# Kernel tuning notes

Hardware: AMD Instinct MI355X
Metric: run time of the kernel (lower is better)

## Reference

```python
import jax, jax.numpy as jnp
import numpy as np
import math

B, N, C = 4, 2048, 768
H = 12
DFF = 4 * C
EPS = 1e-5

def _layernorm(x, gamma, beta):
    mu = jnp.mean(x, axis=-1, keepdims=True)
    var = jnp.var(x, axis=-1, keepdims=True)
    return (x - mu) * jax.lax.rsqrt(var + EPS) * gamma + beta

def setup_inputs() -> dict:
    key = jax.random.key(0)
    ks = jax.random.split(key, 12)
    s = 0.02
    return {
        "x": jax.random.normal(ks[0], (B, N, C), jnp.float32),
        "Wqkv": jax.random.normal(ks[1], (C, 3 * C), jnp.float32) * s,
        "bqkv": jnp.zeros((3 * C,), jnp.float32),
        "Wproj": jax.random.normal(ks[2], (C, C), jnp.float32) * s,
        "bproj": jnp.zeros((C,), jnp.float32),
        "g1": jnp.ones((C,), jnp.float32),
        "b1": jnp.zeros((C,), jnp.float32),
        "g2": jnp.ones((C,), jnp.float32),
        "b2": jnp.zeros((C,), jnp.float32),
        "Wfc1": jax.random.normal(ks[3], (C, DFF), jnp.float32) * s,
        "bfc1": jnp.zeros((DFF,), jnp.float32),
        "Wfc2": jax.random.normal(ks[4], (DFF, C), jnp.float32) * s,
        "bfc2": jnp.zeros((C,), jnp.float32),
    }

def reference(x, Wqkv, bqkv, Wproj, bproj, g1, b1, g2, b2, Wfc1, bfc1, Wfc2, bfc2):
    head_dim = C // H
    qkv = x @ Wqkv + bqkv                      # [B,N,3C]
    q, k, v = jnp.split(qkv, 3, axis=-1)
    # [B,N,C] -> [B,H,N,hd]
    def to_heads(t):
        return t.reshape(B, N, H, head_dim).transpose(0, 2, 1, 3)
    q, k, v = to_heads(q), to_heads(k), to_heads(v)
    attn = jnp.einsum('bhqd,bhkd->bhqk', q, k) / math.sqrt(head_dim)
    attn = jax.nn.softmax(attn, axis=-1)       # dropout p=0 -> identity
    out = jnp.einsum('bhqk,bhkd->bhqd', attn, v)
    out = out.transpose(0, 2, 1, 3).reshape(B, N, C)
    out = out @ Wproj + bproj
    x = _layernorm(x + out, g1, b1)
    h = jax.nn.gelu(x @ Wfc1 + bfc1, approximate=False) @ Wfc2 + bfc2
    x = _layernorm(x + h, g2, b2)
    return x
```

## Files before the change

kernel.cpp:

```cpp
#include <hip/hip_runtime.h>

typedef __bf16 bf16;
typedef __bf16 bf16x2 __attribute__((ext_vector_type(2)));
typedef __bf16 bf16x4 __attribute__((ext_vector_type(4)));
typedef __bf16 bf16x8 __attribute__((ext_vector_type(8)));
typedef float  f32x4  __attribute__((ext_vector_type(4)));
typedef float  f32x16 __attribute__((ext_vector_type(16)));
typedef int    intx4  __attribute__((ext_vector_type(4)));

#define BB 4
#define SEQ 2048
#define CH 768
#define NH 12
#define HD 64
#define DFF 3072
#define MROWS (BB * SEQ)
#define C3 (3 * CH)
#define NBH (BB * NH)

__device__ inline f32x16 mfma32(bf16x8 a, bf16x8 b, f32x16 c) {
    return __builtin_amdgcn_mfma_f32_32x32x16_bf16(a, b, c, 0, 0, 0);
}
__device__ inline f32x4 mfma16(bf16x8 a, bf16x8 b, f32x4 c) {
    return __builtin_amdgcn_mfma_f32_16x16x32_bf16(a, b, c, 0, 0, 0);
}
__device__ inline void gload16(const void* g, void* l) {
    __builtin_amdgcn_global_load_lds((const __attribute__((address_space(1))) void*)g,
                                     (__attribute__((address_space(3))) void*)l, 16, 0, 0);
}
__device__ inline void plswap_i(int& x, int& y) {
    asm volatile("v_permlane32_swap_b32 %0, %1" : "+v"(x), "+v"(y));
}
__device__ inline void plswap_f(float& x, float& y) {
    asm volatile("v_permlane32_swap_b32 %0, %1" : "+v"(x), "+v"(y));
}
__device__ inline int bcast_lo(int v) { int x = v, y = v; plswap_i(x, y); return y; }
__device__ inline int bcast_hi(int v) { int x = v, y = v; plswap_i(x, y); return x; }

__global__ void cvt_f32_bf16(const float* __restrict__ in, bf16* __restrict__ out, int n) {
    int i = (blockIdx.x * blockDim.x + threadIdx.x) * 4;
    if (i + 3 >= n) {
        for (int j = 0; j < 4 && i + j < n; ++j) out[i + j] = (bf16)in[i + j];
        return;
    }
    f32x4 v = *(const f32x4*)&in[i];
    bf16x4 o;
    #pragma unroll
    for (int j = 0; j < 4; ++j) o[j] = (bf16)v[j];
    *(bf16x4*)&out[i] = o;
}

__global__ void transpose_cvt(const float* __restrict__ in, bf16* __restrict__ out, int R, int Cc) {
    __shared__ bf16 t[32][33];
    int tx = threadIdx.x & 31, ty = threadIdx.x >> 5;
    int c0 = blockIdx.x * 32, r0 = blockIdx.y * 32;
    #pragma unroll
    for (int i = 0; i < 32; i += 8)
        t[ty + i][tx] = (bf16)in[(size_t)(r0 + ty + i) * Cc + c0 + tx];
    __syncthreads();
    #pragma unroll
    for (int i = 0; i < 32; i += 8)
        out[(size_t)(c0 + ty + i) * R + r0 + tx] = t[tx][ty + i];
}

__global__ void transpose_v(const bf16* __restrict__ qkvb, bf16* __restrict__ vt) {
    __shared__ bf16 t[32][33];
    int tx = threadIdx.x & 31, ty = threadIdx.x >> 5;
    int n0 = blockIdx.x * 32, d0 = blockIdx.y * 32, bh = blockIdx.z;
    int b = bh / NH, h = bh - b * NH;
    #pragma unroll
    for (int i = 0; i < 32; i += 8)
        t[ty + i][tx] = qkvb[((size_t)b * SEQ + n0 + ty + i) * C3 + 2 * CH + h * HD + d0 + tx];
    __syncthreads();
    #pragma unroll
    for (int i = 0; i < 32; i += 8)
        vt[((size_t)bh * HD + d0 + ty + i) * SEQ + n0 + tx] = t[tx][ty + i];
}

template <int OMODE>
__global__ __launch_bounds__(256) void gemm_bt(const bf16* __restrict__ A,
                                               const bf16* __restrict__ Bt,
                                               const float* __restrict__ bias,
                                               void* __restrict__ Cout,
                                               int M, int N, int K, int lda) {
    __shared__ __align__(16) bf16 As[2][128][32];
    __shared__ __align__(16) bf16 Bs[2][128][32];
    const int nwg = gridDim.x * gridDim.y;
    const int orig = blockIdx.y * gridDim.x + blockIdx.x;
    const int wg = (orig & 7) * (nwg >> 3) + (orig >> 3);
    const int bm = (wg / gridDim.x) * 128, bn = (wg % gridDim.x) * 128;
    const int kbeg = blockIdx.z * K;
    const int tid = threadIdx.x;
    const int lane = tid & 63, w = tid >> 6;
    const int wr = w >> 1, wc = w & 1;
    const int lr = lane & 15, lg = lane >> 4;

    const int srow = tid >> 2, schk = (tid & 3) * 8;
    const bf16* gA0 = A + (size_t)(bm + srow) * lda + kbeg + schk;
    const bf16* gA1 = A + (size_t)(bm + 64 + srow) * lda + kbeg + schk;
    const bf16* gB0 = Bt + (size_t)(bn + srow) * lda + kbeg + schk;
    const bf16* gB1 = Bt + (size_t)(bn + 64 + srow) * lda + kbeg + schk;

    auto stage = [&](int buf, int kofs) {
        gload16(gA0 + kofs, &As[buf][srow][schk]);
        gload16(gA1 + kofs, &As[buf][64 + srow][schk]);
        gload16(gB0 + kofs, &Bs[buf][srow][schk]);
        gload16(gB1 + kofs, &Bs[buf][64 + srow][schk]);
    };

    f32x4 acc[4][4];
    #pragma unroll
    for (int i = 0; i < 4; ++i)
        #pragma unroll
        for (int j = 0; j < 4; ++j) acc[i][j] = (f32x4){0.f, 0.f, 0.f, 0.f};

    stage(0, 0);
    int cur = 0;
    for (int k0 = 0; k0 < K; k0 += 32) {
        __syncthreads();
        if (k0 + 32 < K) stage(cur ^ 1, k0 + 32);
        bf16x8 af[4], bfr[4];
        #pragma unroll
        for (int mi = 0; mi < 4; ++mi)
            af[mi] = *(const bf16x8*)&As[cur][wr * 64 + mi * 16 + lr][lg * 8];
        #pragma unroll
        for (int ni = 0; ni < 4; ++ni)
            bfr[ni] = *(const bf16x8*)&Bs[cur][wc * 64 + ni * 16 + lr][lg * 8];
        #pragma unroll
        for (int mi = 0; mi < 4; ++mi)
            #pragma unroll
            for (int ni = 0; ni < 4; ++ni)
                acc[mi][ni] = mfma16(af[mi], bfr[ni], acc[mi][ni]);
        cur ^= 1;
    }

    #pragma unroll
    for (int mi = 0; mi < 4; ++mi) {
        #pragma unroll
        for (int ni = 0; ni < 4; ++ni) {
            int col = bn + wc * 64 + ni * 16 + lr;
            float bsv = (OMODE == 3) ? 0.f : bias[col];
            #pragma unroll
            for (int r = 0; r < 4; ++r) {
                int row = bm + wr * 64 + mi * 16 + lg * 4 + r;
                float v = acc[mi][ni][r] + bsv;
                if (OMODE == 2) v = 0.5f * v * (1.0f + erff(v * 0.70710678118654752f));
                if (OMODE == 0)
                    ((float*)Cout)[(size_t)row * N + col] = v;
                else if (OMODE == 3)
                    ((bf16*)Cout)[(size_t)blockIdx.z * M * N + (size_t)row * N + col] = (bf16)v;
                else
                    ((bf16*)Cout)[(size_t)row * N + col] = (bf16)v;
            }
        }
    }
}

#define C2F 0.18033688011112f
#define THR2 11.5416f
__global__ __launch_bounds__(256, 3) void attn_kernel(const bf16* __restrict__ qkvb,
                                                      const bf16* __restrict__ vt,
                                                      bf16* __restrict__ outb) {
    __shared__ __align__(16) bf16 Kl[2][64 * 64];
    __shared__ __align__(16) bf16 Vl[2][64 * 64];
    const int tid = threadIdx.x;
    const int w = tid >> 6, lane = tid & 63;
    const int lq = lane & 31;
    const int hi = lane >> 5;
    const int lin = blockIdx.x;
    const int xcd = lin & 7, slot = lin >> 3;
    const int bh = xcd * 6 + (slot >> 4);
    const int qt = slot & 15;
    const int b = bh / NH, h = bh - b * NH;
    const int q0 = qt * 128 + w * 32;

    const bf16* qbase = qkvb + (size_t)b * SEQ * C3 + h * HD;
    const bf16* kbase = qbase + CH;
    const bf16* vbase = vt + (size_t)bh * HD * SEQ;

    const int srow = tid >> 3;
    const int ksc = (tid & 7) ^ (srow & 7);
    const bf16* gk0 = kbase + (size_t)srow * C3 + ksc * 8;
    const bf16* gk1 = kbase + (size_t)(srow + 32) * C3 + ksc * 8;
    const bf16* gv0 = vbase + (size_t)srow * SEQ + ksc * 8;
    const bf16* gv1 = vbase + (size_t)(srow + 32) * SEQ + ksc * 8;
    const int ldst = tid * 8;

    bf16x8 qf[4];
    #pragma unroll
    for (int ks = 0; ks < 4; ++ks)
        qf[ks] = *(const bf16x8*)&qbase[(size_t)(q0 + lq) * C3 + ks * 16 + hi * 8];

    f32x16 o0 = {0.f}, o1 = {0.f};
    float m = -3.0e38f, l = 0.f;

    const int swz = lq & 7;

    auto stage = [&](int buf, int kv0) {
        gload16(gk0 + (size_t)kv0 * C3, &Kl[buf][ldst]);
        gload16(gk1 + (size_t)kv0 * C3, &Kl[buf][2048 + ldst]);
        gload16(gv0 + kv0, &Vl[buf][ldst]);
        gload16(gv1 + kv0, &Vl[buf][2048 + ldst]);
    };

    auto process = [&](const bf16* Kb, const bf16* Vb) {
        f32x16 st0 = {0.f}, st1 = {0.f};
        #pragma unroll
        for (int ks = 0; ks < 4; ++ks) {
            int c = 8 * ((2 * ks + hi) ^ swz);
            bf16x8 k0 = *(const bf16x8*)&Kb[lq * 64 + c];
            bf16x8 k1 = *(const bf16x8*)&Kb[(32 + lq) * 64 + c];
            st0 = mfma32(k0, qf[ks], st0);
            st1 = mfma32(k1, qf[ks], st1);
        }
        float t_[8];
        #pragma unroll
        for (int r = 0; r < 8; ++r)
            t_[r] = fmaxf(fmaxf(st0[r], st0[r + 8]), fmaxf(st1[r], st1[r + 8]));
        #pragma unroll
        for (int r = 0; r < 4; ++r) t_[r] = fmaxf(t_[r], t_[r + 4]);
        float lmax = fmaxf(fmaxf(t_[0], t_[1]), fmaxf(t_[2], t_[3]));
        float mxa = lmax, mxb = lmax;
        plswap_f(mxa, mxb);
        float m2x = fmaxf(mxa, mxb) * C2F;
        if (!__all(m2x <= m + THR2)) {
            float mn = fmaxf(m, m2x);
            float alpha = __builtin_amdgcn_exp2f(m - mn);
            m = mn;
            l *= alpha;
            #pragma unroll
            for (int r = 0; r < 16; ++r) {
                int qr = (r & 3) + 8 * (r >> 2) + 4 * hi;
                float ar = __shfl(alpha, qr);
                o0[r] *= ar;
                o1[r] *= ar;
            }
        }
        bf16x8 pa[4];
        float ps0, ps1;
        {
            float p[16];
            #pragma unroll
            for (int r = 0; r < 16; ++r) p[r] = __builtin_amdgcn_exp2f(fmaf(st0[r], C2F, -m));
            float s0[8];
            #pragma unroll
            for (int r = 0; r < 8; ++r) s0[r] = p[r] + p[r + 8];
            #pragma unroll
            for (int r = 0; r < 4; ++r) s0[r] += s0[r + 4];
            ps0 = (s0[0] + s0[1]) + (s0[2] + s0[3]);
            int a[8];
            #pragma unroll
            for (int i = 0; i < 8; ++i) {
                bf16x2 t2 = {(bf16)p[2 * i], (bf16)p[2 * i + 1]};
                a[i] = __builtin_bit_cast(int, t2);
            }
            intx4 f0 = {bcast_lo(a[0]), bcast_lo(a[1]), bcast_hi(a[2]), bcast_hi(a[3])};
            intx4 f1 = {bcast_lo(a[4]), bcast_lo(a[5]), bcast_hi(a[6]), bcast_hi(a[7])};
            pa[0] = __builtin_bit_cast(bf16x8, f0);
            pa[1] = __builtin_bit_cast(bf16x8, f1);
        }
        {
            float p[16];
            #pragma unroll
            for (int r = 0; r < 16; ++r) p[r] = __builtin_amdgcn_exp2f(fmaf(st1[r], C2F, -m));
            float s0[8];
            #pragma unroll
            for (int r = 0; r < 8; ++r) s0[r] = p[r] + p[r + 8];
            #pragma unroll
            for (int r = 0; r < 4; ++r) s0[r] += s0[r + 4];
            ps1 = (s0[0] + s0[1]) + (s0[2] + s0[3]);
            int a[8];
            #pragma unroll
            for (int i = 0; i < 8; ++i) {
                bf16x2 t2 = {(bf16)p[2 * i], (bf16)p[2 * i + 1]};
                a[i] = __builtin_bit_cast(int, t2);
            }
            intx4 f0 = {bcast_lo(a[0]), bcast_lo(a[1]), bcast_hi(a[2]), bcast_hi(a[3])};
            intx4 f1 = {bcast_lo(a[4]), bcast_lo(a[5]), bcast_hi(a[6]), bcast_hi(a[7])};
            pa[2] = __builtin_bit_cast(bf16x8, f0);
            pa[3] = __builtin_bit_cast(bf16x8, f1);
        }
        float ps = ps0 + ps1;
        float pA = ps, pB = ps;
        plswap_f(pA, pB);
        l += pA + pB;
        #pragma unroll
        for (int c = 0; c < 4; ++c) {
            int cc = 8 * ((2 * c + hi) ^ swz);
            bf16x8 v0 = *(const bf16x8*)&Vb[lq * 64 + cc];
            bf16x8 v1 = *(const bf16x8*)&Vb[(32 + lq) * 64 + cc];
            o0 = mfma32(pa[c], v0, o0);
            o1 = mfma32(pa[c], v1, o1);
        }
    };

    stage(0, 0);
    __syncthreads();
    for (int t = 0; t < 32; t += 2) {
        stage(1, (t + 1) * 64);
        process(Kl[0], Vl[0]);
        __syncthreads();
        stage(0, (t + 2 < 32 ? t + 2 : 31) * 64);
        process(Kl[1], Vl[1]);
        __syncthreads();
    }

    float linv = 1.0f / l;
    const size_t obase = (size_t)b * SEQ * CH + h * HD;
    #pragma unroll
    for (int r = 0; r < 16; ++r) {
        int qr = (r & 3) + 8 * (r >> 2) + 4 * hi;
        float lr_ = __shfl(linv, qr);
        size_t rowo = obase + (size_t)(q0 + qr) * CH;
        outb[rowo + lq] = (bf16)(o0[r] * lr_);
        outb[rowo + 32 + lq] = (bf16)(o1[r] * lr_);
    }
}

template <int XBF16, int OUTF32, int NP>
__global__ __launch_bounds__(256) void add_ln(const void* __restrict__ xin,
                                              const bf16* __restrict__ tp,
                                              const float* __restrict__ bias,
                                              const float* __restrict__ g,
                                              const float* __restrict__ bt,
                                              void* __restrict__ yout) {
    const int row = blockIdx.x;
    const size_t base = (size_t)row * CH;
    const int tid = threadIdx.x;
    float v[3];
    #pragma unroll
    for (int k = 0; k < 3; ++k) {
        int c = tid + k * 256;
        float xv = XBF16 ? (float)((const bf16*)xin)[base + c]
                         : ((const float*)xin)[base + c];
        float acc = xv + bias[c];
        #pragma unroll
        for (int z = 0; z < NP; ++z)
            acc += (float)tp[(size_t)z * MROWS * CH + base + c];
        v[k] = acc;
    }
    __shared__ float red[4];
    float s = v[0] + v[1] + v[2];
    #pragma unroll
    for (int off = 32; off >= 1; off >>= 1) s += __shfl_down(s, off);
    if ((tid & 63) == 0) red[tid >> 6] = s;
    __syncthreads();
    float mean = (red[0] + red[1] + red[2] + red[3]) * (1.0f / 768.0f);
    float q = 0.f;
    #pragma unroll
    for (int k = 0; k < 3; ++k) {
        float d = v[k] - mean;
        q += d * d;
    }
    __syncthreads();
    #pragma unroll
    for (int off = 32; off >= 1; off >>= 1) q += __shfl_down(q, off);
    if ((tid & 63) == 0) red[tid >> 6] = q;
    __syncthreads();
    float var = (red[0] + red[1] + red[2] + red[3]) * (1.0f / 768.0f);
    float rstd = rsqrtf(var + 1e-5f);
    #pragma unroll
    for (int k = 0; k < 3; ++k) {
        int c = tid + k * 256;
        float out = (v[k] - mean) * rstd * g[c] + bt[c];
        if (OUTF32) ((float*)yout)[base + c] = out;
        else        ((bf16*)yout)[base + c] = (bf16)out;
    }
}

extern "C" void kernel_launch(void* const* d_in, const int* in_sizes, int n_in,
                              void* d_out, int out_size, void* d_ws, size_t ws_size,
                              hipStream_t stream) {
    const float* x    = (const float*)d_in[0];
    const float* Wqkv = (const float*)d_in[1];
    const float* bqkv = (const float*)d_in[2];
    const float* Wproj= (const float*)d_in[3];
    const float* bproj= (const float*)d_in[4];
    const float* g1   = (const float*)d_in[5];
    const float* b1   = (const float*)d_in[6];
    const float* g2   = (const float*)d_in[7];
    const float* b2   = (const float*)d_in[8];
    const float* Wfc1 = (const float*)d_in[9];
    const float* bfc1 = (const float*)d_in[10];
    const float* Wfc2 = (const float*)d_in[11];
    const float* bfc2 = (const float*)d_in[12];

    char* ws = (char*)d_ws;
    size_t off = 0;
    auto alloc = [&](size_t bytes) -> void* {
        void* p = ws + off;
        off += (bytes + 255) & ~(size_t)255;
        return p;
    };

    bf16* xb     = (bf16*)alloc((size_t)MROWS * CH * 2);
    bf16* WqkvT  = (bf16*)alloc((size_t)C3 * CH * 2);
    bf16* WprojT = (bf16*)alloc((size_t)CH * CH * 2);
    bf16* Wfc1T  = (bf16*)alloc((size_t)DFF * CH * 2);
    bf16* Wfc2T  = (bf16*)alloc((size_t)CH * DFF * 2);
    bf16* qkvb   = (bf16*)alloc((size_t)MROWS * C3 * 2);
    bf16* vtb    = (bf16*)alloc((size_t)NBH * HD * SEQ * 2);
    bf16* attnb  = (bf16*)alloc((size_t)MROWS * CH * 2);
    bf16* tmpP   = (bf16*)alloc((size_t)4 * MROWS * CH * 2);
    bf16* y1b    = (bf16*)alloc((size_t)MROWS * CH * 2);
    bf16* hb     = (bf16*)alloc((size_t)MROWS * DFF * 2);

    cvt_f32_bf16<<<(MROWS * CH / 4 + 255) / 256, 256, 0, stream>>>(x, xb, MROWS * CH);
    transpose_cvt<<<dim3(C3 / 32, CH / 32), 256, 0, stream>>>(Wqkv, WqkvT, CH, C3);
    transpose_cvt<<<dim3(CH / 32, CH / 32), 256, 0, stream>>>(Wproj, WprojT, CH, CH);
    transpose_cvt<<<dim3(DFF / 32, CH / 32), 256, 0, stream>>>(Wfc1, Wfc1T, CH, DFF);
    transpose_cvt<<<dim3(CH / 32, DFF / 32), 256, 0, stream>>>(Wfc2, Wfc2T, DFF, CH);
    gemm_bt<1><<<dim3(C3 / 128, MROWS / 128), 256, 0, stream>>>(xb, WqkvT, bqkv, qkvb, MROWS, C3, CH, CH);
    transpose_v<<<dim3(SEQ / 32, HD / 32, NBH), 256, 0, stream>>>(qkvb, vtb);
    attn_kernel<<<768, 256, 0, stream>>>(qkvb, vtb, attnb);
    gemm_bt<3><<<dim3(CH / 128, MROWS / 128, 2), 256, 0, stream>>>(attnb, WprojT, nullptr, tmpP, MROWS, CH, CH / 2, CH);
    add_ln<0, 0, 2><<<MROWS, 256, 0, stream>>>(x, tmpP, bproj, g1, b1, y1b);
    gemm_bt<2><<<dim3(DFF / 128, MROWS / 128), 256, 0, stream>>>(y1b, Wfc1T, bfc1, hb, MROWS, DFF, CH, CH);
    gemm_bt<3><<<dim3(CH / 128, MROWS / 128, 4), 256, 0, stream>>>(hb, Wfc2T, nullptr, tmpP, MROWS, CH, DFF / 4, DFF);
    add_ln<1, 1, 4><<<MROWS, 256, 0, stream>>>(y1b, tmpP, bfc2, g2, b2, (float*)d_out);
}
```

Before: 310.3 us.

## Split attention KV range across two blocks and merge with log-sum-exp combine

Attention now runs a 768x2 grid where each block handles half of the key/value sequence. Each block writes a normalized partial output plus a per-row log-sum-exp, and a new combine kernel merges the two halves into the head-interleaved layout. This doubles the number of blocks so more of the GPU is busy, at the cost of an extra kernel launch and more global traffic for the partials. Separately, the FC2 split-K factor drops from 4 to 2, which cuts partial-sum traffic in the following layernorm.

```diff
diff --git a/kernel.cpp b/kernel.cpp
--- a/kernel.cpp
+++ b/kernel.cpp
@@ -17,6 +17,7 @@
 #define MROWS (BB * SEQ)
 #define C3 (3 * CH)
 #define NBH (BB * NH)
+#define RTOT (NBH * SEQ)
 
 __device__ inline f32x16 mfma32(bf16x8 a, bf16x8 b, f32x16 c) {
     return __builtin_amdgcn_mfma_f32_32x32x16_bf16(a, b, c, 0, 0, 0);
@@ -158,9 +159,12 @@
 
 #define C2F 0.18033688011112f
 #define THR2 11.5416f
+#define KVHALF 1024
+#define NTILE 16
 __global__ __launch_bounds__(256, 3) void attn_kernel(const bf16* __restrict__ qkvb,
                                                       const bf16* __restrict__ vt,
-                                                      bf16* __restrict__ outb) {
+                                                      bf16* __restrict__ po,
+                                                      float* __restrict__ lse) {
     __shared__ __align__(16) bf16 Kl[2][64 * 64];
     __shared__ __align__(16) bf16 Vl[2][64 * 64];
     const int tid = threadIdx.x;
@@ -168,11 +172,13 @@
     const int lq = lane & 31;
     const int hi = lane >> 5;
     const int lin = blockIdx.x;
+    const int z = blockIdx.y;
     const int xcd = lin & 7, slot = lin >> 3;
     const int bh = xcd * 6 + (slot >> 4);
     const int qt = slot & 15;
     const int b = bh / NH, h = bh - b * NH;
     const int q0 = qt * 128 + w * 32;
+    const int kvbase = z * KVHALF;
 
     const bf16* qbase = qkvb + (size_t)b * SEQ * C3 + h * HD;
     const bf16* kbase = qbase + CH;
@@ -294,27 +300,52 @@
         }
     };
 
-    stage(0, 0);
-    __syncthreads();
-    for (int t = 0; t < 32; t += 2) {
-        stage(1, (t + 1) * 64);
+    stage(0, kvbase);
+    __syncthreads();
+    for (int t = 0; t < NTILE; t += 2) {
+        stage(1, kvbase + (t + 1) * 64);
         process(Kl[0], Vl[0]);
         __syncthreads();
-        stage(0, (t + 2 < 32 ? t + 2 : 31) * 64);
+        stage(0, kvbase + (t + 2 < NTILE ? t + 2 : NTILE - 1) * 64);
         process(Kl[1], Vl[1]);
         __syncthreads();
     }
 
     float linv = 1.0f / l;
-    const size_t obase = (size_t)b * SEQ * CH + h * HD;
+    const size_t rbase = (size_t)z * NBH * SEQ + (size_t)bh * SEQ + q0;
     #pragma unroll
     for (int r = 0; r < 16; ++r) {
         int qr = (r & 3) + 8 * (r >> 2) + 4 * hi;
         float lr_ = __shfl(linv, qr);
-        size_t rowo = obase + (size_t)(q0 + qr) * CH;
-        outb[rowo + lq] = (bf16)(o0[r] * lr_);
-        outb[rowo + 32 + lq] = (bf16)(o1[r] * lr_);
-    }
+        size_t ro = (rbase + qr) * 64;
+        po[ro + lq] = (bf16)(o0[r] * lr_);
+        po[ro + 32 + lq] = (bf16)(o1[r] * lr_);
+    }
+    if (hi == 0)
+        lse[rbase + lq] = m + __builtin_amdgcn_logf(l);
+}
+
+__global__ __launch_bounds__(256) void attn_combine(const bf16* __restrict__ po,
+                                                    const float* __restrict__ lse,
+                                                    bf16* __restrict__ attnb) {
+    const int tid = threadIdx.x;
+    const int row = blockIdx.x * 32 + (tid >> 3);
+    const int d0 = (tid & 7) * 8;
+    const int bh = row >> 11, s = row & 2047;
+    const int b = bh / NH, h = bh - b * NH;
+    float l0 = lse[row], l1 = lse[RTOT + row];
+    float L = fmaxf(l0, l1);
+    float w0 = __builtin_amdgcn_exp2f(l0 - L);
+    float w1 = __builtin_amdgcn_exp2f(l1 - L);
+    float wn = 1.0f / (w0 + w1);
+    w0 *= wn; w1 *= wn;
+    bf16x8 p0 = *(const bf16x8*)&po[(size_t)row * 64 + d0];
+    bf16x8 p1 = *(const bf16x8*)&po[((size_t)RTOT + row) * 64 + d0];
+    bf16x8 o;
+    #pragma unroll
+    for (int j = 0; j < 8; ++j)
+        o[j] = (bf16)((float)p0[j] * w0 + (float)p1[j] * w1);
+    *(bf16x8*)&attnb[((size_t)b * SEQ + s) * CH + h * HD + d0] = o;
 }
 
 template <int XBF16, int OUTF32, int NP>
@@ -404,6 +435,8 @@
     bf16* tmpP   = (bf16*)alloc((size_t)4 * MROWS * CH * 2);
     bf16* y1b    = (bf16*)alloc((size_t)MROWS * CH * 2);
     bf16* hb     = (bf16*)alloc((size_t)MROWS * DFF * 2);
+    float* lsebuf= (float*)alloc((size_t)2 * RTOT * 4);
+    bf16* po = tmpP;
 
     cvt_f32_bf16<<<(MROWS * CH / 4 + 255) / 256, 256, 0, stream>>>(x, xb, MROWS * CH);
     transpose_cvt<<<dim3(C3 / 32, CH / 32), 256, 0, stream>>>(Wqkv, WqkvT, CH, C3);
@@ -412,10 +445,11 @@
     transpose_cvt<<<dim3(CH / 32, DFF / 32), 256, 0, stream>>>(Wfc2, Wfc2T, DFF, CH);
     gemm_bt<1><<<dim3(C3 / 128, MROWS / 128), 256, 0, stream>>>(xb, WqkvT, bqkv, qkvb, MROWS, C3, CH, CH);
     transpose_v<<<dim3(SEQ / 32, HD / 32, NBH), 256, 0, stream>>>(qkvb, vtb);
-    attn_kernel<<<768, 256, 0, stream>>>(qkvb, vtb, attnb);
+    attn_kernel<<<dim3(768, 2), 256, 0, stream>>>(qkvb, vtb, po, lsebuf);
+    attn_combine<<<RTOT / 32, 256, 0, stream>>>(po, lsebuf, attnb);
     gemm_bt<3><<<dim3(CH / 128, MROWS / 128, 2), 256, 0, stream>>>(attnb, WprojT, nullptr, tmpP, MROWS, CH, CH / 2, CH);
     add_ln<0, 0, 2><<<MROWS, 256, 0, stream>>>(x, tmpP, bproj, g1, b1, y1b);
     gemm_bt<2><<<dim3(DFF / 128, MROWS / 128), 256, 0, stream>>>(y1b, Wfc1T, bfc1, hb, MROWS, DFF, CH, CH);
-    gemm_bt<3><<<dim3(CH / 128, MROWS / 128, 4), 256, 0, stream>>>(hb, Wfc2T, nullptr, tmpP, MROWS, CH, DFF / 4, DFF);
-    add_ln<1, 1, 4><<<MROWS, 256, 0, stream>>>(y1b, tmpP, bfc2, g2, b2, (float*)d_out);
-}
+    gemm_bt<3><<<dim3(CH / 128, MROWS / 128, 2), 256, 0, stream>>>(hb, Wfc2T, nullptr, tmpP, MROWS, CH, DFF / 2, DFF);
+    add_ln<1, 1, 2><<<MROWS, 256, 0, stream>>>(y1b, tmpP, bfc2, g2, b2, (float*)d_out);
+}
```

Result: no change. 310.3 us (+0.0%).

## Fuse prep conversions, deepen attention K/V pipeline, halve FC2 split-K

Applied to the files above, without the earlier changes.

Merges the input cast and four weight transpose-casts into one launch, dispatching on block index. Attention now uses four K/V LDS buffers, prefetching two tiles ahead with one barrier per pair of tiles instead of two. FC2 split-K drops from 4 to 2 partitions, reducing partial-sum traffic in the final add+layernorm. The doubled LDS may lower attention occupancy.

```diff
diff --git a/kernel.cpp b/kernel.cpp
--- a/kernel.cpp
+++ b/kernel.cpp
@@ -37,30 +37,40 @@
 __device__ inline int bcast_lo(int v) { int x = v, y = v; plswap_i(x, y); return y; }
 __device__ inline int bcast_hi(int v) { int x = v, y = v; plswap_i(x, y); return x; }
 
-__global__ void cvt_f32_bf16(const float* __restrict__ in, bf16* __restrict__ out, int n) {
-    int i = (blockIdx.x * blockDim.x + threadIdx.x) * 4;
-    if (i + 3 >= n) {
-        for (int j = 0; j < 4 && i + j < n; ++j) out[i + j] = (bf16)in[i + j];
+__global__ __launch_bounds__(256) void prep_kernel(
+    const float* __restrict__ x, bf16* __restrict__ xb,
+    const float* __restrict__ Wqkv, bf16* __restrict__ WqkvT,
+    const float* __restrict__ Wproj, bf16* __restrict__ WprojT,
+    const float* __restrict__ Wfc1, bf16* __restrict__ Wfc1T,
+    const float* __restrict__ Wfc2, bf16* __restrict__ Wfc2T) {
+    __shared__ bf16 t[32][33];
+    int bid = blockIdx.x;
+    if (bid < 6144) {
+        int i = (bid * 256 + threadIdx.x) * 4;
+        f32x4 v = *(const f32x4*)&x[i];
+        bf16x4 o;
+        #pragma unroll
+        for (int j = 0; j < 4; ++j) o[j] = (bf16)v[j];
+        *(bf16x4*)&xb[i] = o;
         return;
     }
-    f32x4 v = *(const f32x4*)&in[i];
-    bf16x4 o;
-    #pragma unroll
-    for (int j = 0; j < 4; ++j) o[j] = (bf16)v[j];
-    *(bf16x4*)&out[i] = o;
-}
-
-__global__ void transpose_cvt(const float* __restrict__ in, bf16* __restrict__ out, int R, int Cc) {
-    __shared__ bf16 t[32][33];
+    bid -= 6144;
+    const float* src;
+    bf16* dst;
+    int R, Cc, wT;
+    if (bid < 1728)      { src = Wqkv;  dst = WqkvT;  R = CH;  Cc = C3;  wT = 72; }
+    else if (bid < 2304) { bid -= 1728; src = Wproj; dst = WprojT; R = CH;  Cc = CH;  wT = 24; }
+    else if (bid < 4608) { bid -= 2304; src = Wfc1;  dst = Wfc1T;  R = CH;  Cc = DFF; wT = 96; }
+    else                 { bid -= 4608; src = Wfc2;  dst = Wfc2T;  R = DFF; Cc = CH;  wT = 24; }
     int tx = threadIdx.x & 31, ty = threadIdx.x >> 5;
-    int c0 = blockIdx.x * 32, r0 = blockIdx.y * 32;
+    int c0 = (bid % wT) * 32, r0 = (bid / wT) * 32;
     #pragma unroll
     for (int i = 0; i < 32; i += 8)
-        t[ty + i][tx] = (bf16)in[(size_t)(r0 + ty + i) * Cc + c0 + tx];
+        t[ty + i][tx] = (bf16)src[(size_t)(r0 + ty + i) * Cc + c0 + tx];
     __syncthreads();
     #pragma unroll
     for (int i = 0; i < 32; i += 8)
-        out[(size_t)(c0 + ty + i) * R + r0 + tx] = t[tx][ty + i];
+        dst[(size_t)(c0 + ty + i) * R + r0 + tx] = t[tx][ty + i];
 }
 
 __global__ void transpose_v(const bf16* __restrict__ qkvb, bf16* __restrict__ vt) {
@@ -161,8 +171,8 @@
 __global__ __launch_bounds__(256, 3) void attn_kernel(const bf16* __restrict__ qkvb,
                                                       const bf16* __restrict__ vt,
                                                       bf16* __restrict__ outb) {
-    __shared__ __align__(16) bf16 Kl[2][64 * 64];
-    __shared__ __align__(16) bf16 Vl[2][64 * 64];
+    __shared__ __align__(16) bf16 Kl[4][64 * 64];
+    __shared__ __align__(16) bf16 Vl[4][64 * 64];
     const int tid = threadIdx.x;
     const int w = tid >> 6, lane = tid & 63;
     const int lq = lane & 31;
@@ -295,13 +305,15 @@
     };
 
     stage(0, 0);
+    stage(1, 64);
     __syncthreads();
     for (int t = 0; t < 32; t += 2) {
-        stage(1, (t + 1) * 64);
-        process(Kl[0], Vl[0]);
-        __syncthreads();
-        stage(0, (t + 2 < 32 ? t + 2 : 31) * 64);
-        process(Kl[1], Vl[1]);
+        if (t + 2 < 32) {
+            stage((t + 2) & 3, (t + 2) * 64);
+            stage((t + 3) & 3, (t + 3) * 64);
+        }
+        process(Kl[t & 3], Vl[t & 3]);
+        process(Kl[(t + 1) & 3], Vl[(t + 1) & 3]);
         __syncthreads();
     }
 
@@ -401,21 +413,18 @@
     bf16* qkvb   = (bf16*)alloc((size_t)MROWS * C3 * 2);
     bf16* vtb    = (bf16*)alloc((size_t)NBH * HD * SEQ * 2);
     bf16* attnb  = (bf16*)alloc((size_t)MROWS * CH * 2);
-    bf16* tmpP   = (bf16*)alloc((size_t)4 * MROWS * CH * 2);
+    bf16* tmpP   = (bf16*)alloc((size_t)2 * MROWS * CH * 2);
     bf16* y1b    = (bf16*)alloc((size_t)MROWS * CH * 2);
     bf16* hb     = (bf16*)alloc((size_t)MROWS * DFF * 2);
 
-    cvt_f32_bf16<<<(MROWS * CH / 4 + 255) / 256, 256, 0, stream>>>(x, xb, MROWS * CH);
-    transpose_cvt<<<dim3(C3 / 32, CH / 32), 256, 0, stream>>>(Wqkv, WqkvT, CH, C3);
-    transpose_cvt<<<dim3(CH / 32, CH / 32), 256, 0, stream>>>(Wproj, WprojT, CH, CH);
-    transpose_cvt<<<dim3(DFF / 32, CH / 32), 256, 0, stream>>>(Wfc1, Wfc1T, CH, DFF);
-    transpose_cvt<<<dim3(CH / 32, DFF / 32), 256, 0, stream>>>(Wfc2, Wfc2T, DFF, CH);
+    prep_kernel<<<13056, 256, 0, stream>>>(x, xb, Wqkv, WqkvT, Wproj, WprojT,
+                                           Wfc1, Wfc1T, Wfc2, Wfc2T);
     gemm_bt<1><<<dim3(C3 / 128, MROWS / 128), 256, 0, stream>>>(xb, WqkvT, bqkv, qkvb, MROWS, C3, CH, CH);
     transpose_v<<<dim3(SEQ / 32, HD / 32, NBH), 256, 0, stream>>>(qkvb, vtb);
     attn_kernel<<<768, 256, 0, stream>>>(qkvb, vtb, attnb);
     gemm_bt<3><<<dim3(CH / 128, MROWS / 128, 2), 256, 0, stream>>>(attnb, WprojT, nullptr, tmpP, MROWS, CH, CH / 2, CH);
     add_ln<0, 0, 2><<<MROWS, 256, 0, stream>>>(x, tmpP, bproj, g1, b1, y1b);
     gemm_bt<2><<<dim3(DFF / 128, MROWS / 128), 256, 0, stream>>>(y1b, Wfc1T, bfc1, hb, MROWS, DFF, CH, CH);
-    gemm_bt<3><<<dim3(CH / 128, MROWS / 128, 4), 256, 0, stream>>>(hb, Wfc2T, nullptr, tmpP, MROWS, CH, DFF / 4, DFF);
-    add_ln<1, 1, 4><<<MROWS, 256, 0, stream>>>(y1b, tmpP, bfc2, g2, b2, (float*)d_out);
-}
+    gemm_bt<3><<<dim3(CH / 128, MROWS / 128, 2), 256, 0, stream>>>(hb, Wfc2T, nullptr, tmpP, MROWS, CH, DFF / 2, DFF);
+    add_ln<1, 1, 2><<<MROWS, 256, 0, stream>>>(y1b, tmpP, bfc2, g2, b2, (float*)d_out);
+}
```

After: 310.0 us. Within noise of the previous version (-0.1%).
